# Kernel optimization log

Measured on AMD Instinct MI355X. Metric: run time of the kernel, lower is better.

## Reference

```python
import jax, jax.numpy as jnp
import numpy as np

B, T, D, H, S, PM = 2048, 128, 32, 256, 39, 12


def setup_inputs() -> dict:
    key = jax.random.key(0)
    ks = jax.random.split(key, 20)
    s = 0.05
    return {
        "x": jax.random.normal(ks[0], (B, T, D), jnp.float32),
        "latlons": jax.random.normal(ks[1], (B, 2), jnp.float32),
        "yearly_aggs": jax.random.normal(ks[2], (B, 37), jnp.float32),
        "pred_month": jax.random.uniform(ks[3], (B, PM), jnp.float32),
        # EA-LSTM cell parameters (Linear stores weight as [out,in])
        "Wf_i": jax.random.normal(ks[4], (H, D), jnp.float32) * s,
        "Wf_h": jax.random.normal(ks[5], (H, H), jnp.float32) * s,
        "bf_h": jnp.zeros((H,), jnp.float32),
        "Wu": jax.random.normal(ks[6], (H, S), jnp.float32) * s,
        "bu": jnp.zeros((H,), jnp.float32),
        "Wg_i": jax.random.normal(ks[7], (H, D), jnp.float32) * s,
        "Wg_h": jax.random.normal(ks[8], (H, H), jnp.float32) * s,
        "bg_h": jnp.zeros((H,), jnp.float32),
        "Wo_i": jax.random.normal(ks[9], (H, D), jnp.float32) * s,
        "Wo_h": jax.random.normal(ks[10], (H, H), jnp.float32) * s,
        "bo_h": jnp.zeros((H,), jnp.float32),
        # dense head: [268 -> 256 -> 1], no nonlinearity between layers (as in source)
        "Wd0": jax.random.normal(ks[11], (256, H + PM), jnp.float32) * s,
        "bd0": jnp.zeros((256,), jnp.float32),
        "Wd1": jax.random.normal(ks[12], (1, 256), jnp.float32) * s,
        "bd1": jnp.zeros((1,), jnp.float32),
    }


def reference(x, latlons, yearly_aggs, pred_month,
              Wf_i, Wf_h, bf_h, Wu, bu,
              Wg_i, Wg_h, bg_h, Wo_i, Wo_h, bo_h,
              Wd0, bd0, Wd1, bd1):
    x_s = jnp.concatenate([latlons, yearly_aggs], axis=-1)  # [B,S]
    i_gate = jax.nn.sigmoid(x_s @ Wu.T + bu)  # [B,H], static input gate

    # Precompute the input-to-gate projections for all timesteps (one big GEMM each)
    pf = jnp.einsum('btd,hd->tbh', x, Wf_i)  # [T,B,H]
    pg = jnp.einsum('btd,hd->tbh', x, Wg_i)
    po = jnp.einsum('btd,hd->tbh', x, Wo_i)

    h0 = jnp.zeros((x.shape[0], Wf_h.shape[0]), x.dtype)
    c0 = jnp.zeros_like(h0)

    def step(carry, inp):
        h, c = carry
        pf_t, pg_t, po_t = inp
        f = jax.nn.sigmoid(pf_t + h @ Wf_h.T + bf_h)
        g = jnp.tanh(pg_t + h @ Wg_h.T + bg_h)
        o = jax.nn.sigmoid(po_t + h @ Wo_h.T + bo_h)
        c1 = f * c + i_gate * g
        h1 = o * jnp.tanh(c1)
        return (h1, c1), None

    (h_last, _), _ = jax.lax.scan(step, (h0, c0), (pf, pg, po))

    # only the last hidden state feeds the dense head (dropout p=0 -> identity)
    z = jnp.concatenate([h_last, pred_month], axis=-1)  # [B, H+12]
    z = z @ Wd0.T + bd0
    z = z @ Wd1.T + bd1
    return z  # [B,1]
```

## Files before the change

kernel.cpp:

```cpp
#include <hip/hip_runtime.h>

typedef __bf16 bf16x8 __attribute__((ext_vector_type(8)));
typedef float  f32x4  __attribute__((ext_vector_type(4)));
typedef int    v4i    __attribute__((ext_vector_type(4)));

#define LOG2E 1.4426950408889634f

__device__ __forceinline__ float fexp(float x){ return __builtin_amdgcn_exp2f(x * LOG2E); }
__device__ __forceinline__ float sigm(float x){ return __builtin_amdgcn_rcpf(1.0f + fexp(-x)); }
__device__ __forceinline__ float ftanh(float x){
  float r = __builtin_amdgcn_rcpf(1.0f + __builtin_amdgcn_exp2f(-2.0f*LOG2E*x));
  return 2.0f*r - 1.0f;
}
__device__ __forceinline__ f32x4 MFMA(bf16x8 a, bf16x8 b, f32x4 c){
  return __builtin_amdgcn_mfma_f32_16x16x32_bf16(a, b, c, 0, 0, 0);
}
#define BC(w) __builtin_bit_cast(v4i, (w))

#define GRP_A(LEAD, A_, KT_) asm volatile(LEAD                  \
    "v_mfma_f32_16x16x32_bf16 %0, %6, %7, %0\n\t"               \
    "v_mfma_f32_16x16x32_bf16 %1, %6, %8, %1\n\t"               \
    "v_mfma_f32_16x16x32_bf16 %2, %6, %9, %2\n\t"               \
    "v_mfma_f32_16x16x32_bf16 %3, %6, %10, %3\n\t"              \
    "v_mfma_f32_16x16x32_bf16 %4, %6, %11, %4\n\t"              \
    "v_mfma_f32_16x16x32_bf16 %5, %6, %12, %5\n\t"              \
    "s_nop 3"                                                   \
    : "+v"(acc0),"+v"(acc1),"+v"(acc2),"+v"(acc3),"+v"(acc4),"+v"(acc5) \
    : "v"(A_), "a"(awf[(KT_)]),"a"(awf[(KT_)+5]),"a"(awf[(KT_)+10]),    \
      "a"(awf[(KT_)+15]),"a"(awf[(KT_)+20]),"a"(awf[(KT_)+25]))

#define GRP_V(A_, O_) asm volatile(                             \
    "v_mfma_f32_16x16x32_bf16 %0, %6, %7, %0\n\t"               \
    "v_mfma_f32_16x16x32_bf16 %1, %6, %8, %1\n\t"               \
    "v_mfma_f32_16x16x32_bf16 %2, %6, %9, %2\n\t"               \
    "v_mfma_f32_16x16x32_bf16 %3, %6, %10, %3\n\t"              \
    "v_mfma_f32_16x16x32_bf16 %4, %6, %11, %4\n\t"              \
    "v_mfma_f32_16x16x32_bf16 %5, %6, %12, %5\n\t"              \
    "s_nop 3"                                                   \
    : "+v"(acc0),"+v"(acc1),"+v"(acc2),"+v"(acc3),"+v"(acc4),"+v"(acc5) \
    : "v"(A_), "v"(wvf[(O_)]),"v"(wvf[(O_)+2]),"v"(wvf[(O_)+4]),        \
      "v"(wvf[(O_)+6]),"v"(wvf[(O_)+8]),"v"(wvf[(O_)+10]))

#define GRP_L3(AC0, AC1, AC2, A_, ADDR_, O0, O1, O2) asm volatile(  \
    "ds_read_b128 %3, %7 offset:" O0 "\n\t"                     \
    "ds_read_b128 %4, %7 offset:" O1 "\n\t"                     \
    "ds_read_b128 %5, %7 offset:" O2 "\n\t"                     \
    "s_waitcnt lgkmcnt(0)\n\t"                                  \
    "v_mfma_f32_16x16x32_bf16 %0, %6, %3, %0\n\t"               \
    "v_mfma_f32_16x16x32_bf16 %1, %6, %4, %1\n\t"               \
    "v_mfma_f32_16x16x32_bf16 %2, %6, %5, %2\n\t"               \
    "s_nop 3"                                                   \
    : "+v"(AC0),"+v"(AC1),"+v"(AC2),                            \
      "=&v"(t0),"=&v"(t1),"=&v"(t2)                             \
    : "v"(A_), "v"(ADDR_))

__global__ void
__attribute__((amdgpu_flat_work_group_size(512,512), amdgpu_waves_per_eu(2,2)))
ealstm_kernel(
    const float* __restrict__ x,      const float* __restrict__ latlons,
    const float* __restrict__ yearly, const float* __restrict__ pm,
    const float* __restrict__ Wf_i, const float* __restrict__ Wf_h, const float* __restrict__ bf_h,
    const float* __restrict__ Wu,   const float* __restrict__ bu,
    const float* __restrict__ Wg_i, const float* __restrict__ Wg_h, const float* __restrict__ bg_h,
    const float* __restrict__ Wo_i, const float* __restrict__ Wo_h, const float* __restrict__ bo_h,
    const float* __restrict__ Wd0,  const float* __restrict__ bd0,
    const float* __restrict__ Wd1,  const float* __restrict__ bd1,
    float* __restrict__ out)
{
  __shared__ __align__(16) __bf16 hbuf[2][16*264];
  __shared__ __align__(16) __bf16 xbuf[2][16*40];
  __shared__ __align__(16) __bf16 wlds[2*48*512];
  __shared__ __align__(16) float  xs[16*64];

  const int tid  = threadIdx.x;
  const int w    = tid >> 6;
  const int lane = tid & 63;
  const int q    = lane >> 4;
  const int l    = lane & 15;
  const int wgb  = blockIdx.x * 8;

  const float* Wh[3] = {Wf_h, Wg_h, Wo_h};
  const float* Wi[3] = {Wf_i, Wg_i, Wo_i};
  const float* bH[3] = {bf_h, bg_h, bo_h};

  for(int idx = tid; idx < 16*64; idx += 512){
    int m = idx >> 6, k = idx & 63;
    float v = 0.0f;
    if(m < 8){
      int b = wgb + m;
      if(k < 2) v = latlons[b*2 + k];
      else if(k < 39) v = yearly[b*37 + (k-2)];
    }
    xs[idx] = v;
  }
  for(int idx = tid; idx < 2*16*264; idx += 512) ((__bf16*)hbuf)[idx] = (__bf16)0.0f;
  {
    int buf = tid >> 8, r = 8 + ((tid >> 5) & 7), c = tid & 31;
    xbuf[buf][r*40 + c] = (__bf16)0.0f;
  }
  if(tid < 256){
    int m = tid >> 5, k = tid & 31;
    xbuf[0][m*40 + k] = (__bf16)x[(size_t)(wgb + m)*4096 + k];
  }
  for(int grp = tid; grp < 2*48*64; grp += 512){
    int frag = grp >> 6, ln = grp & 63;
    int kk = frag / 48, f2 = frag % 48;
    int g = f2 >> 4, nt = f2 & 15;
    int q2 = ln >> 4, l2 = ln & 15;
    int cc = nt*16 + l2;
    const float* p = (kk == 0) ? (Wh[g] + cc*256 + 224 + q2*8)
                               : (Wi[g] + cc*32  + q2*8);
    bf16x8 v;
    #pragma unroll
    for(int j=0;j<8;j++) v[j] = (__bf16)p[j];
    *(bf16x8*)&wlds[frag*512 + ln*8] = v;
  }

  v4i awf[30];
  v4i wvf[12];
  #pragma unroll
  for(int f = 0; f < 42; f++){
    int gn = f / 7, kt = f % 7;
    int g = gn >> 1, n = gn & 1;
    int cc = w*32 + n*16 + l;
    const float* p = Wh[g] + cc*256 + kt*32 + q*8;
    f32x4 v0 = *(const f32x4*)p;
    f32x4 v1 = *(const f32x4*)(p + 4);
    bf16x8 v;
    v[0]=(__bf16)v0[0]; v[1]=(__bf16)v0[1]; v[2]=(__bf16)v0[2]; v[3]=(__bf16)v0[3];
    v[4]=(__bf16)v1[0]; v[5]=(__bf16)v1[1]; v[6]=(__bf16)v1[2]; v[7]=(__bf16)v1[3];
    if(kt < 5) awf[gn*5 + kt] = BC(v);
    else       wvf[gn*2 + (kt-5)] = BC(v);
    if((f % 7) == 6) asm volatile("" ::: "memory");
  }
  float bgn[6];
  #pragma unroll
  for(int gn=0; gn<6; gn++) bgn[gn] = bH[gn>>1][w*32 + (gn&1)*16 + l];

  const int  srcl = lane & 31;
  const bool lo   = lane < 32;
  const int  qq4  = (q & 1) * 4;
  const int  colw = w*32 + ((lane & 32) >> 1) + l;
  const unsigned waddr0 = (unsigned)(unsigned long long)&wlds[(0*48 + w*2)*512 + lane*8];
  const unsigned waddr1 = (unsigned)(unsigned long long)&wlds[(1*48 + w*2)*512 + lane*8];

  __syncthreads();

  f32x4 igv;
  {
    float bu0 = bu[w*32 + l], bu1 = bu[w*32 + 16 + l];
    f32x4 iga0 = {bu0,bu0,bu0,bu0};
    f32x4 iga1 = {bu1,bu1,bu1,bu1};
    #pragma unroll
    for(int kt=0; kt<2; kt++){
      bf16x8 a;
      const float* xr = &xs[l*64 + kt*32 + q*8];
      #pragma unroll
      for(int j=0;j<8;j++) a[j] = (__bf16)xr[j];
      #pragma unroll
      for(int n=0;n<2;n++){
        int cc = w*32 + n*16 + l;
        bf16x8 b;
        #pragma unroll
        for(int j=0;j<8;j++){
          int k = kt*32 + q*8 + j;
          b[j] = (__bf16)((k < 39) ? Wu[cc*39 + k] : 0.0f);
        }
        if(n == 0) iga0 = MFMA(a, b, iga0); else iga1 = MFMA(a, b, iga1);
      }
    }
    #pragma unroll
    for(int i=0;i<4;i++){
      float s0 = sigm(iga0[i]);
      float s1 = __shfl(sigm(iga1[i]), srcl);
      igv[i] = lo ? s0 : s1;
    }
  }

  f32x4 cst = {0.f, 0.f, 0.f, 0.f};

#define LSTM_STEP(T_, CUR_)                                                     \
  {                                                                             \
    const int t = (T_);                                                         \
       \
    if(w == 7 && lane < 32 && t < 127){                                         \
      int row = lane >> 2, c0 = (lane & 3) * 8;                                 \
      const float* xp = x + (size_t)(wgb + row)*4096 + (t+1)*32 + c0;           \
      f32x4 v0 = *(const f32x4*)xp;                                             \
      f32x4 v1 = *(const f32x4*)(xp + 4);                                       \
      bf16x8 v;                                                                 \
      v[0]=(__bf16)v0[0]; v[1]=(__bf16)v0[1]; v[2]=(__bf16)v0[2]; v[3]=(__bf16)v0[3]; \
      v[4]=(__bf16)v1[0]; v[5]=(__bf16)v1[1]; v[6]=(__bf16)v1[2]; v[7]=(__bf16)v1[3]; \
      *(bf16x8*)&xbuf[(CUR_) ^ 1][row*40 + c0] = v;                             \
    }                                                                           \
    asm volatile("" ::: "memory");                                              \
    f32x4 bc0 = {bgn[0],bgn[0],bgn[0],bgn[0]};                                  \
    f32x4 bc1 = {bgn[1],bgn[1],bgn[1],bgn[1]};                                  \
    f32x4 bc2 = {bgn[2],bgn[2],bgn[2],bgn[2]};                                  \
    f32x4 bc3 = {bgn[3],bgn[3],bgn[3],bgn[3]};                                  \
    f32x4 bc4 = {bgn[4],bgn[4],bgn[4],bgn[4]};                                  \
    f32x4 bc5 = {bgn[5],bgn[5],bgn[5],bgn[5]};                                  \
    v4i acc0 = BC(bc0), acc1 = BC(bc1), acc2 = BC(bc2);                         \
    v4i acc3 = BC(bc3), acc4 = BC(bc4), acc5 = BC(bc5);                         \
    v4i t0, t1, t2;                                                             \
    const __bf16* hb = hbuf[CUR_];                                              \
    { v4i a = BC(*(const bf16x8*)&hb[l*264 + 0*32 + q*8]); GRP_A("s_nop 3\n\t", a, 0); } \
    { v4i a = BC(*(const bf16x8*)&hb[l*264 + 1*32 + q*8]); GRP_A("", a, 1); }   \
    { v4i a = BC(*(const bf16x8*)&hb[l*264 + 2*32 + q*8]); GRP_A("", a, 2); }   \
    { v4i a = BC(*(const bf16x8*)&hb[l*264 + 3*32 + q*8]); GRP_A("", a, 3); }   \
    { v4i a = BC(*(const bf16x8*)&hb[l*264 + 4*32 + q*8]); GRP_A("", a, 4); }   \
    { v4i a = BC(*(const bf16x8*)&hb[l*264 + 5*32 + q*8]); GRP_V(a, 0); }       \
    { v4i a = BC(*(const bf16x8*)&hb[l*264 + 6*32 + q*8]); GRP_V(a, 1); }       \
    { v4i a = BC(*(const bf16x8*)&hb[l*264 + 7*32 + q*8]);                      \
      GRP_L3(acc0, acc2, acc4, a, waddr0, "0", "16384", "32768");               \
      GRP_L3(acc1, acc3, acc5, a, waddr0, "1024", "17408", "33792"); }          \
    { v4i a = BC(*(const bf16x8*)&xbuf[CUR_][l*40 + q*8]);                      \
      GRP_L3(acc0, acc2, acc4, a, waddr1, "0", "16384", "32768");               \
      GRP_L3(acc1, acc3, acc5, a, waddr1, "1024", "17408", "33792"); }          \
    asm volatile("s_nop 7\n\ts_nop 7\n\ts_nop 7"                                \
      : "+v"(acc0),"+v"(acc1),"+v"(acc2),"+v"(acc3),"+v"(acc4),"+v"(acc5));     \
    f32x4 a0 = __builtin_bit_cast(f32x4, acc0);                                 \
    f32x4 a1 = __builtin_bit_cast(f32x4, acc1);                                 \
    f32x4 a2 = __builtin_bit_cast(f32x4, acc2);                                 \
    f32x4 a3 = __builtin_bit_cast(f32x4, acc3);                                 \
    f32x4 a4 = __builtin_bit_cast(f32x4, acc4);                                 \
    f32x4 a5 = __builtin_bit_cast(f32x4, acc5);                                 \
    _Pragma("unroll")                                                           \
    for(int i=0;i<4;i++){                                                       \
      float f1 = __shfl(a1[i], srcl);                                           \
      float g1 = __shfl(a3[i], srcl);                                           \
      float o1 = __shfl(a5[i], srcl);                                           \
      float fv = sigm (lo ? a0[i] : f1);                                        \
      float gv = ftanh(lo ? a2[i] : g1);                                        \
      float ov = sigm (lo ? a4[i] : o1);                                        \
      float cc = fv * cst[i] + igv[i] * gv;                                     \
      cst[i] = cc;                                                              \
      hbuf[(CUR_) ^ 1][(qq4 + i)*264 + colw] = (__bf16)(ov * ftanh(cc));        \
    }                                                                           \
    __syncthreads();                                                            \
  }

  #pragma unroll 1
  for(int tt = 0; tt < 64; tt++){
    LSTM_STEP(2*tt,     0)
    LSTM_STEP(2*tt + 1, 1)
  }
#undef LSTM_STEP

  f32x4 hd[2];
  { f32x4 z4 = {0.f,0.f,0.f,0.f}; hd[0] = z4; hd[1] = z4; }
  #pragma unroll 2
  for(int kt=0; kt<8; kt++){
    bf16x8 a = *(const bf16x8*)&hbuf[0][l*264 + kt*32 + q*8];
    #pragma unroll
    for(int n=0;n<2;n++){
      int cc = w*32 + n*16 + l;
      const float* p = Wd0 + cc*268 + kt*32 + q*8;
      bf16x8 b;
      #pragma unroll
      for(int j=0;j<8;j++) b[j] = (__bf16)p[j];
      hd[n] = MFMA(a, b, hd[n]);
    }
  }
  {
    bf16x8 a;
    #pragma unroll
    for(int j=0;j<8;j++){
      int k2 = q*8 + j;
      a[j] = (__bf16)((l < 8 && k2 < 12) ? pm[(size_t)(wgb + l)*12 + k2] : 0.0f);
    }
    #pragma unroll
    for(int n=0;n<2;n++){
      int cc = w*32 + n*16 + l;
      bf16x8 b;
      #pragma unroll
      for(int j=0;j<8;j++){
        int k2 = q*8 + j;
        b[j] = (__bf16)((k2 < 12) ? Wd0[cc*268 + 256 + k2] : 0.0f);
      }
      hd[n] = MFMA(a, b, hd[n]);
    }
  }
  float* z1 = (float*)wlds;
  #pragma unroll
  for(int n=0;n<2;n++){
    int cc = w*32 + n*16 + l;
    float bb = bd0[cc];
    #pragma unroll
    for(int i=0;i<4;i++) z1[(q*4 + i)*264 + cc] = hd[n][i] + bb;
  }
  __syncthreads();
  if(tid < 256){
    int row = tid >> 5, seg = tid & 31;
    const float* zr = &z1[row*264 + seg*8];
    const float* wr = Wd1 + seg*8;
    float s = 0.0f;
    #pragma unroll
    for(int j=0;j<8;j++) s += zr[j] * wr[j];
    s += __shfl_xor(s, 1);
    s += __shfl_xor(s, 2);
    s += __shfl_xor(s, 4);
    s += __shfl_xor(s, 8);
    s += __shfl_xor(s, 16);
    if(seg == 0) out[wgb + row] = s + bd1[0];
  }
}

extern "C" void kernel_launch(void* const* d_in, const int* in_sizes, int n_in,
                              void* d_out, int out_size, void* d_ws, size_t ws_size,
                              hipStream_t stream) {
  const float* x       = (const float*)d_in[0];
  const float* latlons = (const float*)d_in[1];
  const float* yearly  = (const float*)d_in[2];
  const float* pm      = (const float*)d_in[3];
  const float* Wf_i    = (const float*)d_in[4];
  const float* Wf_h    = (const float*)d_in[5];
  const float* bf_h    = (const float*)d_in[6];
  const float* Wu      = (const float*)d_in[7];
  const float* bu      = (const float*)d_in[8];
  const float* Wg_i    = (const float*)d_in[9];
  const float* Wg_h    = (const float*)d_in[10];
  const float* bg_h    = (const float*)d_in[11];
  const float* Wo_i    = (const float*)d_in[12];
  const float* Wo_h    = (const float*)d_in[13];
  const float* bo_h    = (const float*)d_in[14];
  const float* Wd0     = (const float*)d_in[15];
  const float* bd0     = (const float*)d_in[16];
  const float* Wd1     = (const float*)d_in[17];
  const float* bd1     = (const float*)d_in[18];

  ealstm_kernel<<<dim3(256), dim3(512), 0, stream>>>(
      x, latlons, yearly, pm,
      Wf_i, Wf_h, bf_h, Wu, bu,
      Wg_i, Wg_h, bg_h, Wo_i, Wo_h, bo_h,
      Wd0, bd0, Wd1, bd1,
      (float*)d_out);
}
```

Measured before the change: 413.9 us.

## Restructure LSTM step: tiled h layout, fused LDS reads, x prefetch, bias post-add

Changes the hidden-state LDS layout from padded rows to k-tile-major 16x32 blocks, merges the last two K-slices' LDS weight reads and MFMAs into one asm block, and prefetches x for step t+2 into registers so the global load latency is off the critical path. It also moves the gate bias add into the activation stage, replaces __syncthreads with an explicit lgkmcnt wait plus s_barrier, and forces the register-resident weights into AGPRs. The aim is to shorten the serial per-timestep latency. The cost is higher register pressure and more reliance on hand-written asm hazard handling.

```diff
diff --git a/kernel.cpp b/kernel.cpp
--- a/kernel.cpp
+++ b/kernel.cpp
@@ -41,18 +41,39 @@
     : "v"(A_), "v"(wvf[(O_)]),"v"(wvf[(O_)+2]),"v"(wvf[(O_)+4]),        \
       "v"(wvf[(O_)+6]),"v"(wvf[(O_)+8]),"v"(wvf[(O_)+10]))
 
-#define GRP_L3(AC0, AC1, AC2, A_, ADDR_, O0, O1, O2) asm volatile(  \
-    "ds_read_b128 %3, %7 offset:" O0 "\n\t"                     \
-    "ds_read_b128 %4, %7 offset:" O1 "\n\t"                     \
-    "ds_read_b128 %5, %7 offset:" O2 "\n\t"                     \
+#define GRP_LX(A7_, AX_) asm volatile(                          \
+    "ds_read_b128 %6, %14\n\t"                                  \
+    "ds_read_b128 %7, %14 offset:1024\n\t"                      \
+    "ds_read_b128 %8, %14 offset:16384\n\t"                     \
+    "ds_read_b128 %9, %14 offset:17408\n\t"                     \
+    "ds_read_b128 %10, %14 offset:32768\n\t"                    \
+    "ds_read_b128 %11, %14 offset:33792\n\t"                    \
     "s_waitcnt lgkmcnt(0)\n\t"                                  \
-    "v_mfma_f32_16x16x32_bf16 %0, %6, %3, %0\n\t"               \
-    "v_mfma_f32_16x16x32_bf16 %1, %6, %4, %1\n\t"               \
-    "v_mfma_f32_16x16x32_bf16 %2, %6, %5, %2\n\t"               \
+    "v_mfma_f32_16x16x32_bf16 %0, %12, %6, %0\n\t"              \
+    "v_mfma_f32_16x16x32_bf16 %1, %12, %7, %1\n\t"              \
+    "v_mfma_f32_16x16x32_bf16 %2, %12, %8, %2\n\t"              \
+    "v_mfma_f32_16x16x32_bf16 %3, %12, %9, %3\n\t"              \
+    "v_mfma_f32_16x16x32_bf16 %4, %12, %10, %4\n\t"             \
+    "v_mfma_f32_16x16x32_bf16 %5, %12, %11, %5\n\t"             \
+    "ds_read_b128 %6, %15\n\t"                                  \
+    "ds_read_b128 %7, %15 offset:1024\n\t"                      \
+    "ds_read_b128 %8, %15 offset:16384\n\t"                     \
+    "ds_read_b128 %9, %15 offset:17408\n\t"                     \
+    "ds_read_b128 %10, %15 offset:32768\n\t"                    \
+    "ds_read_b128 %11, %15 offset:33792\n\t"                    \
+    "s_waitcnt lgkmcnt(0)\n\t"                                  \
+    "v_mfma_f32_16x16x32_bf16 %0, %13, %6, %0\n\t"              \
+    "v_mfma_f32_16x16x32_bf16 %1, %13, %7, %1\n\t"              \
+    "v_mfma_f32_16x16x32_bf16 %2, %13, %8, %2\n\t"              \
+    "v_mfma_f32_16x16x32_bf16 %3, %13, %9, %3\n\t"              \
+    "v_mfma_f32_16x16x32_bf16 %4, %13, %10, %4\n\t"             \
+    "v_mfma_f32_16x16x32_bf16 %5, %13, %11, %5\n\t"             \
     "s_nop 3"                                                   \
-    : "+v"(AC0),"+v"(AC1),"+v"(AC2),                            \
-      "=&v"(t0),"=&v"(t1),"=&v"(t2)                             \
-    : "v"(A_), "v"(ADDR_))
+    : "+v"(acc0),"+v"(acc1),"+v"(acc2),"+v"(acc3),"+v"(acc4),"+v"(acc5), \
+      "=&v"(t0),"=&v"(t1),"=&v"(t2),"=&v"(t3),"=&v"(t4),"=&v"(t5)        \
+    : "v"(A7_), "v"(AX_), "v"(waddr0), "v"(waddr1))
+
+#define BARRIER() asm volatile("s_waitcnt lgkmcnt(0)\n\ts_barrier" ::: "memory")
 
 __global__ void
 __attribute__((amdgpu_flat_work_group_size(512,512), amdgpu_waves_per_eu(2,2)))
@@ -67,7 +88,7 @@
     const float* __restrict__ Wd1,  const float* __restrict__ bd1,
     float* __restrict__ out)
 {
-  __shared__ __align__(16) __bf16 hbuf[2][16*264];
+  __shared__ __align__(16) __bf16 hbuf[2][4096];
   __shared__ __align__(16) __bf16 xbuf[2][16*40];
   __shared__ __align__(16) __bf16 wlds[2*48*512];
   __shared__ __align__(16) float  xs[16*64];
@@ -81,7 +102,6 @@
 
   const float* Wh[3] = {Wf_h, Wg_h, Wo_h};
   const float* Wi[3] = {Wf_i, Wg_i, Wo_i};
-  const float* bH[3] = {bf_h, bg_h, bo_h};
 
   for(int idx = tid; idx < 16*64; idx += 512){
     int m = idx >> 6, k = idx & 63;
@@ -93,7 +113,7 @@
     }
     xs[idx] = v;
   }
-  for(int idx = tid; idx < 2*16*264; idx += 512) ((__bf16*)hbuf)[idx] = (__bf16)0.0f;
+  for(int idx = tid; idx < 2*4096; idx += 512) ((__bf16*)hbuf)[idx] = (__bf16)0.0f;
   {
     int buf = tid >> 8, r = 8 + ((tid >> 5) & 7), c = tid & 31;
     xbuf[buf][r*40 + c] = (__bf16)0.0f;
@@ -116,33 +136,14 @@
     *(bf16x8*)&wlds[frag*512 + ln*8] = v;
   }
 
-  v4i awf[30];
-  v4i wvf[12];
-  #pragma unroll
-  for(int f = 0; f < 42; f++){
-    int gn = f / 7, kt = f % 7;
-    int g = gn >> 1, n = gn & 1;
-    int cc = w*32 + n*16 + l;
-    const float* p = Wh[g] + cc*256 + kt*32 + q*8;
-    f32x4 v0 = *(const f32x4*)p;
-    f32x4 v1 = *(const f32x4*)(p + 4);
-    bf16x8 v;
-    v[0]=(__bf16)v0[0]; v[1]=(__bf16)v0[1]; v[2]=(__bf16)v0[2]; v[3]=(__bf16)v0[3];
-    v[4]=(__bf16)v1[0]; v[5]=(__bf16)v1[1]; v[6]=(__bf16)v1[2]; v[7]=(__bf16)v1[3];
-    if(kt < 5) awf[gn*5 + kt] = BC(v);
-    else       wvf[gn*2 + (kt-5)] = BC(v);
-    if((f % 7) == 6) asm volatile("" ::: "memory");
-  }
-  float bgn[6];
-  #pragma unroll
-  for(int gn=0; gn<6; gn++) bgn[gn] = bH[gn>>1][w*32 + (gn&1)*16 + l];
-
   const int  srcl = lane & 31;
   const bool lo   = lane < 32;
   const int  qq4  = (q & 1) * 4;
   const int  colw = w*32 + ((lane & 32) >> 1) + l;
+  const int  hwb  = (colw >> 5)*512 + qq4*32 + ((colw >> 3) & 3)*8 + (colw & 7);
   const unsigned waddr0 = (unsigned)(unsigned long long)&wlds[(0*48 + w*2)*512 + lane*8];
-  const unsigned waddr1 = (unsigned)(unsigned long long)&wlds[(1*48 + w*2)*512 + lane*8];
+  const unsigned waddr1 = waddr0 + 49152u;
+  const float b3f = bf_h[colw], b3g = bg_h[colw], b3o = bo_h[colw];
 
   __syncthreads();
 
@@ -177,46 +178,80 @@
     }
   }
 
+  v4i wvf[12];
+  #pragma unroll
+  for(int f = 0; f < 12; f++){
+    int gn = f >> 1, kt = 5 + (f & 1);
+    int g = gn >> 1, n = gn & 1;
+    int cc = w*32 + n*16 + l;
+    const float* p = Wh[g] + cc*256 + kt*32 + q*8;
+    f32x4 v0 = *(const f32x4*)p;
+    f32x4 v1 = *(const f32x4*)(p + 4);
+    bf16x8 v;
+    v[0]=(__bf16)v0[0]; v[1]=(__bf16)v0[1]; v[2]=(__bf16)v0[2]; v[3]=(__bf16)v0[3];
+    v[4]=(__bf16)v1[0]; v[5]=(__bf16)v1[1]; v[6]=(__bf16)v1[2]; v[7]=(__bf16)v1[3];
+    wvf[f] = BC(v);
+    if((f & 3) == 3) asm volatile("" ::: "memory");
+  }
+  v4i awf[30];
+  #pragma unroll
+  for(int f = 0; f < 30; f++){
+    int gn = f / 5, kt = f % 5;
+    int g = gn >> 1, n = gn & 1;
+    int cc = w*32 + n*16 + l;
+    const float* p = Wh[g] + cc*256 + kt*32 + q*8;
+    f32x4 v0 = *(const f32x4*)p;
+    f32x4 v1 = *(const f32x4*)(p + 4);
+    bf16x8 v;
+    v[0]=(__bf16)v0[0]; v[1]=(__bf16)v0[1]; v[2]=(__bf16)v0[2]; v[3]=(__bf16)v0[3];
+    v[4]=(__bf16)v1[0]; v[5]=(__bf16)v1[1]; v[6]=(__bf16)v1[2]; v[7]=(__bf16)v1[3];
+    asm("" : "=a"(awf[f]) : "0"(BC(v)));
+    if((f % 5) == 4) asm volatile("" ::: "memory");
+  }
+
   f32x4 cst = {0.f, 0.f, 0.f, 0.f};
+
+  const int xri = (lane >> 2)*40 + (lane & 3)*8;
+  const float* xbase = x + (size_t)(wgb + (lane >> 2))*4096 + (lane & 3)*8;
+  f32x4 pv0 = {0.f,0.f,0.f,0.f}, pv1 = {0.f,0.f,0.f,0.f};
+  if(w == 7 && lane < 32){
+    pv0 = *(const f32x4*)(xbase + 32);
+    pv1 = *(const f32x4*)(xbase + 36);
+  }
+  asm volatile("" ::: "memory");
 
 #define LSTM_STEP(T_, CUR_)                                                     \
   {                                                                             \
-    const int t = (T_);                                                         \
-       \
-    if(w == 7 && lane < 32 && t < 127){                                         \
-      int row = lane >> 2, c0 = (lane & 3) * 8;                                 \
-      const float* xp = x + (size_t)(wgb + row)*4096 + (t+1)*32 + c0;           \
-      f32x4 v0 = *(const f32x4*)xp;                                             \
-      f32x4 v1 = *(const f32x4*)(xp + 4);                                       \
-      bf16x8 v;                                                                 \
-      v[0]=(__bf16)v0[0]; v[1]=(__bf16)v0[1]; v[2]=(__bf16)v0[2]; v[3]=(__bf16)v0[3]; \
-      v[4]=(__bf16)v1[0]; v[5]=(__bf16)v1[1]; v[6]=(__bf16)v1[2]; v[7]=(__bf16)v1[3]; \
-      *(bf16x8*)&xbuf[(CUR_) ^ 1][row*40 + c0] = v;                             \
+      \
+      \
+    if(w == 7 && lane < 32){                                                    \
+      if((T_) < 127){                                                           \
+        bf16x8 v;                                                               \
+        v[0]=(__bf16)pv0[0]; v[1]=(__bf16)pv0[1]; v[2]=(__bf16)pv0[2]; v[3]=(__bf16)pv0[3]; \
+        v[4]=(__bf16)pv1[0]; v[5]=(__bf16)pv1[1]; v[6]=(__bf16)pv1[2]; v[7]=(__bf16)pv1[3]; \
+        *(bf16x8*)&xbuf[(CUR_) ^ 1][xri] = v;                                   \
+      }                                                                         \
+      if((T_) < 126){                                                           \
+        pv0 = *(const f32x4*)(xbase + ((T_)+2)*32);                             \
+        pv1 = *(const f32x4*)(xbase + ((T_)+2)*32 + 4);                         \
+      }                                                                         \
     }                                                                           \
     asm volatile("" ::: "memory");                                              \
-    f32x4 bc0 = {bgn[0],bgn[0],bgn[0],bgn[0]};                                  \
-    f32x4 bc1 = {bgn[1],bgn[1],bgn[1],bgn[1]};                                  \
-    f32x4 bc2 = {bgn[2],bgn[2],bgn[2],bgn[2]};                                  \
-    f32x4 bc3 = {bgn[3],bgn[3],bgn[3],bgn[3]};                                  \
-    f32x4 bc4 = {bgn[4],bgn[4],bgn[4],bgn[4]};                                  \
-    f32x4 bc5 = {bgn[5],bgn[5],bgn[5],bgn[5]};                                  \
-    v4i acc0 = BC(bc0), acc1 = BC(bc1), acc2 = BC(bc2);                         \
-    v4i acc3 = BC(bc3), acc4 = BC(bc4), acc5 = BC(bc5);                         \
-    v4i t0, t1, t2;                                                             \
+    f32x4 z4 = {0.f,0.f,0.f,0.f};                                               \
+    v4i acc0 = BC(z4), acc1 = BC(z4), acc2 = BC(z4);                            \
+    v4i acc3 = BC(z4), acc4 = BC(z4), acc5 = BC(z4);                            \
+    v4i t0, t1, t2, t3, t4, t5;                                                 \
     const __bf16* hb = hbuf[CUR_];                                              \
-    { v4i a = BC(*(const bf16x8*)&hb[l*264 + 0*32 + q*8]); GRP_A("s_nop 3\n\t", a, 0); } \
-    { v4i a = BC(*(const bf16x8*)&hb[l*264 + 1*32 + q*8]); GRP_A("", a, 1); }   \
-    { v4i a = BC(*(const bf16x8*)&hb[l*264 + 2*32 + q*8]); GRP_A("", a, 2); }   \
-    { v4i a = BC(*(const bf16x8*)&hb[l*264 + 3*32 + q*8]); GRP_A("", a, 3); }   \
-    { v4i a = BC(*(const bf16x8*)&hb[l*264 + 4*32 + q*8]); GRP_A("", a, 4); }   \
-    { v4i a = BC(*(const bf16x8*)&hb[l*264 + 5*32 + q*8]); GRP_V(a, 0); }       \
-    { v4i a = BC(*(const bf16x8*)&hb[l*264 + 6*32 + q*8]); GRP_V(a, 1); }       \
-    { v4i a = BC(*(const bf16x8*)&hb[l*264 + 7*32 + q*8]);                      \
-      GRP_L3(acc0, acc2, acc4, a, waddr0, "0", "16384", "32768");               \
-      GRP_L3(acc1, acc3, acc5, a, waddr0, "1024", "17408", "33792"); }          \
-    { v4i a = BC(*(const bf16x8*)&xbuf[CUR_][l*40 + q*8]);                      \
-      GRP_L3(acc0, acc2, acc4, a, waddr1, "0", "16384", "32768");               \
-      GRP_L3(acc1, acc3, acc5, a, waddr1, "1024", "17408", "33792"); }          \
+    { v4i a = BC(*(const bf16x8*)&hb[0*512 + l*32 + q*8]); GRP_A("s_nop 3\n\t", a, 0); } \
+    { v4i a = BC(*(const bf16x8*)&hb[1*512 + l*32 + q*8]); GRP_A("", a, 1); }   \
+    { v4i a = BC(*(const bf16x8*)&hb[2*512 + l*32 + q*8]); GRP_A("", a, 2); }   \
+    { v4i a = BC(*(const bf16x8*)&hb[3*512 + l*32 + q*8]); GRP_A("", a, 3); }   \
+    { v4i a = BC(*(const bf16x8*)&hb[4*512 + l*32 + q*8]); GRP_A("", a, 4); }   \
+    { v4i a = BC(*(const bf16x8*)&hb[5*512 + l*32 + q*8]); GRP_V(a, 0); }       \
+    { v4i a = BC(*(const bf16x8*)&hb[6*512 + l*32 + q*8]); GRP_V(a, 1); }       \
+    { v4i a7 = BC(*(const bf16x8*)&hb[7*512 + l*32 + q*8]);                     \
+      v4i ax = BC(*(const bf16x8*)&xbuf[CUR_][l*40 + q*8]);                     \
+      GRP_LX(a7, ax); }                                                         \
     asm volatile("s_nop 7\n\ts_nop 7\n\ts_nop 7"                                \
       : "+v"(acc0),"+v"(acc1),"+v"(acc2),"+v"(acc3),"+v"(acc4),"+v"(acc5));     \
     f32x4 a0 = __builtin_bit_cast(f32x4, acc0);                                 \
@@ -230,14 +265,14 @@
       float f1 = __shfl(a1[i], srcl);                                           \
       float g1 = __shfl(a3[i], srcl);                                           \
       float o1 = __shfl(a5[i], srcl);                                           \
-      float fv = sigm (lo ? a0[i] : f1);                                        \
-      float gv = ftanh(lo ? a2[i] : g1);                                        \
-      float ov = sigm (lo ? a4[i] : o1);                                        \
+      float fv = sigm ((lo ? a0[i] : f1) + b3f);                                \
+      float gv = ftanh((lo ? a2[i] : g1) + b3g);                                \
+      float ov = sigm ((lo ? a4[i] : o1) + b3o);                                \
       float cc = fv * cst[i] + igv[i] * gv;                                     \
       cst[i] = cc;                                                              \
-      hbuf[(CUR_) ^ 1][(qq4 + i)*264 + colw] = (__bf16)(ov * ftanh(cc));        \
+      hbuf[(CUR_) ^ 1][hwb + i*32] = (__bf16)(ov * ftanh(cc));                  \
     }                                                                           \
-    __syncthreads();                                                            \
+    BARRIER();                                                                  \
   }
 
   #pragma unroll 1
@@ -251,7 +286,7 @@
   { f32x4 z4 = {0.f,0.f,0.f,0.f}; hd[0] = z4; hd[1] = z4; }
   #pragma unroll 2
   for(int kt=0; kt<8; kt++){
-    bf16x8 a = *(const bf16x8*)&hbuf[0][l*264 + kt*32 + q*8];
+    bf16x8 a = *(const bf16x8*)&hbuf[0][kt*512 + l*32 + q*8];
     #pragma unroll
     for(int n=0;n<2;n++){
       int cc = w*32 + n*16 + l;
```

Measured after the change: 354.0 us. 14.5% less time.
